# Optimization experiments

Hardware: AMD Instinct MI355X
Metric: run time of the kernel (lower is better)

## Reference

```python
import jax, jax.numpy as jnp
import numpy as np

B, NV, CIN, C = 1, 40000, 128, 64
D, H, W = 19, 200, 176  # sparse_shape = output_shape[1:4] + [1,0,0]
EPS = 1e-3
DN = ('NCDHW', 'OIDHW', 'NCDHW')


def setup_inputs():
    key = jax.random.key(0)
    ks = jax.random.split(key, 12)
    vf = jax.random.normal(ks[0], (NV, CIN), jnp.float32)
    bi = jnp.zeros((NV, 1), jnp.int32)
    zi = jax.random.randint(ks[1], (NV, 1), 0, D, jnp.int32)
    yi = jax.random.randint(ks[2], (NV, 1), 0, H, jnp.int32)
    xi = jax.random.randint(ks[3], (NV, 1), 0, W, jnp.int32)
    coors = jnp.concatenate([bi, zi, yi, xi], axis=1)  # [batch, z, y, x]
    s = 0.05
    w_sub1 = jax.random.normal(ks[4], (C, CIN, 3, 3, 3), jnp.float32) * s
    w_down1 = jax.random.normal(ks[5], (C, C, 3, 1, 1), jnp.float32) * s
    w_sub2 = jax.random.normal(ks[6], (C, C, 3, 3, 3), jnp.float32) * s
    w_sub3 = jax.random.normal(ks[7], (C, C, 3, 3, 3), jnp.float32) * s
    w_down2 = jax.random.normal(ks[8], (C, C, 3, 1, 1), jnp.float32) * s
    bn_gamma = 1.0 + 0.1 * jax.random.normal(ks[9], (5, C), jnp.float32)
    bn_beta = 0.1 * jax.random.normal(ks[10], (5, C), jnp.float32)
    bn_mean = 0.1 * jax.random.normal(ks[11], (5, C), jnp.float32)
    bn_var = jnp.ones((5, C), jnp.float32)
    return dict(voxel_features=vf, coors=coors, batch_size=1,
                w_sub1=w_sub1, w_down1=w_down1, w_sub2=w_sub2, w_sub3=w_sub3,
                w_down2=w_down2, bn_gamma=bn_gamma, bn_beta=bn_beta,
                bn_mean=bn_mean, bn_var=bn_var)


def _conv(x, w, stride, pad):
    return jax.lax.conv_general_dilated(x, w, stride, pad, dimension_numbers=DN)


def _bnrelu(x, i, mask, g, b, m, v):
    # eval-mode BN on active sites only (inactive sites stay exactly zero -> mask)
    inv = jax.lax.rsqrt(v[i] + EPS)
    y = (x - m[i][None, :, None, None, None]) * (g[i] * inv)[None, :, None, None, None] \
        + b[i][None, :, None, None, None]
    return jnp.maximum(y, 0.0) * mask


def _forward(voxel_features, coors, batch_size, w_sub1, w_down1, w_sub2, w_sub3,
             w_down2, bn_gamma, bn_beta, bn_mean, bn_var):
    bi, zi, yi, xi = coors[:, 0], coors[:, 1], coors[:, 2], coors[:, 3]
    # scn.InputLayer: scatter (sum duplicates) active voxel features into dense grid
    dense = jnp.zeros((batch_size, D, H, W, CIN), voxel_features.dtype)
    dense = dense.at[bi, zi, yi, xi].add(voxel_features)
    x = jnp.transpose(dense, (0, 4, 1, 2, 3))  # NCDHW
    mask = jnp.zeros((batch_size, D, H, W), voxel_features.dtype)
    mask = mask.at[bi, zi, yi, xi].set(1.0)[:, None]  # [B,1,D,H,W] active sites
    ones_k = jnp.ones((1, 1, 3, 1, 1), x.dtype)
    pad1 = ((1, 1), (1, 1), (1, 1))
    bn = (bn_gamma, bn_beta, bn_mean, bn_var)
    # SubmanifoldConvolution(128->64, k3) + BNReLU : output only at active sites
    x = _bnrelu(_conv(x, w_sub1, (1, 1, 1), pad1) * mask, 0, mask, *bn)
    # Convolution 64->64 kernel (3,1,1) stride (2,1,1): new active set = any input in window
    x = _conv(x, w_down1, (2, 1, 1), 'VALID')
    mask = (_conv(mask, ones_k, (2, 1, 1), 'VALID') > 0).astype(x.dtype)
    x = _bnrelu(x, 1, mask, *bn)
    # two more submanifold convs
    x = _bnrelu(_conv(x, w_sub2, (1, 1, 1), pad1) * mask, 2, mask, *bn)
    x = _bnrelu(_conv(x, w_sub3, (1, 1, 1), pad1) * mask, 3, mask, *bn)
    # second strided conv
    x = _conv(x, w_down2, (2, 1, 1), 'VALID')
    mask = (_conv(mask, ones_k, (2, 1, 1), 'VALID') > 0).astype(x.dtype)
    x = _bnrelu(x, 4, mask, *bn)
    # SparseToDense then view(N, C*D, H, W)
    Nb, Cc, Dd, Hh, Ww = x.shape
    return x.reshape(Nb, Cc * Dd, Hh, Ww)


def reference(voxel_features, coors, batch_size, w_sub1, w_down1, w_sub2, w_sub3,
              w_down2, bn_gamma, bn_beta, bn_mean, bn_var):
    return _forward(voxel_features, coors, batch_size, w_sub1, w_down1, w_sub2,
                    w_sub3, w_down2, bn_gamma, bn_beta, bn_mean, bn_var)
```

## Files before the change

kernel.cpp:

```cpp
#include <hip/hip_runtime.h>

typedef float floatx4 __attribute__((ext_vector_type(4)));
typedef _Float16 f16x8 __attribute__((ext_vector_type(8)));

#define D0_ 19
#define H0_ 200
#define W0_ 176
#define HW_ (H0_*W0_)
#define NCELL0 (D0_*HW_)
#define D1_ 9
#define NCELL1 (D1_*HW_)
#define D2_ 4
#define NCELL2 (D2_*HW_)
#define NV_ 40000
#define CAP0 40000
#define CAP1 80000
#define CAP2 140800
#define EPS_ 1e-3f

typedef __attribute__((address_space(1))) const unsigned int* gas_t;
typedef __attribute__((address_space(3))) unsigned int* las_t;

__device__ __forceinline__ short f2h(float f){
    _Float16 h = (_Float16)f;
    short s; __builtin_memcpy(&s, &h, 2); return s;
}

__device__ __forceinline__ void repack_one(const float* w, short* Bout, int i,
                                           int KCsrc, int kshift, int NSP){
    int k = i >> 6, n = i & 63;
    int j = k >> kshift;
    int ci = k & (KCsrc - 1);
    short val = f2h(w[(n * KCsrc + ci) * NSP + j]);
    int chunk = k >> 5, lanehi = (k >> 3) & 3, jj = k & 7;
    int nt = n >> 4, lane = lanehi * 16 + (n & 15);
    Bout[((chunk * 4 + nt) * 64 + lane) * 8 + jj] = val;
}

#define RP1 (3456*64)
#define RP2 (1728*64)
#define RPD (192*64)

__global__ void k_prep(const float* w1, const float* w2, const float* w3,
                       const float* wd1, const float* wd2,
                       short* B1, short* B2, short* B3, short* Bd1, short* Bd2,
                       const float* g, const float* b, const float* m, const float* v,
                       float* scale, float* shift){
    int i = blockIdx.x * 256 + threadIdx.x;
    if (i < RP1){ repack_one(w1, B1, i, 128, 7, 27); return; }
    i -= RP1;
    if (i < RP2){ repack_one(w2, B2, i, 64, 6, 27); return; }
    i -= RP2;
    if (i < RP2){ repack_one(w3, B3, i, 64, 6, 27); return; }
    i -= RP2;
    if (i < RPD){ repack_one(wd1, Bd1, i, 64, 6, 3); return; }
    i -= RPD;
    if (i < RPD){ repack_one(wd2, Bd2, i, 64, 6, 3); return; }
    i -= RPD;
    if (i < 5*64){
        float s = g[i] / sqrtf(v[i] + EPS_);
        scale[i] = s;
        shift[i] = b[i] - m[i] * s;
    }
}
#define PREP_TOT (RP1 + 2*RP2 + 2*RPD + 5*64)

__global__ void k_count(const int* coors, int* cntg){
    int v = blockIdx.x * 256 + threadIdx.x;
    if (v >= NV_) return;
    int z = coors[v*4+1], y = coors[v*4+2], x = coors[v*4+3];
    atomicAdd(&cntg[(z*H0_ + y)*W0_ + x], 1);
}

__device__ __forceinline__ int blk_rank(bool act, int* cnt, int& r_out){
    unsigned long long mask = __ballot(act);
    int lane = threadIdx.x & 63, wid = threadIdx.x >> 6;
    int wrank = __popcll(mask & ((1ull << lane) - 1));
    __shared__ int ws[4];
    __shared__ int blkbase;
    if (lane == 0) ws[wid] = __popcll(mask);
    __syncthreads();
    if (threadIdx.x == 0){
        int t0 = ws[0], t1 = ws[1], t2 = ws[2], t3 = ws[3];
        int tot = t0 + t1 + t2 + t3;
        blkbase = tot ? atomicAdd(cnt, tot) : 0;
        ws[0] = 0; ws[1] = t0; ws[2] = t0 + t1; ws[3] = t0 + t1 + t2;
    }
    __syncthreads();
    r_out = blkbase + ws[wid] + wrank;
    return 0;
}

__global__ void k_compact0(const int* cntg, int* idx0, int* list0, int* cnt0){
    int c = blockIdx.x * 256 + threadIdx.x;
    bool act = (c < NCELL0) && (cntg[c] > 0);
    int r; blk_rank(act, cnt0, r);
    if (c >= NCELL0) return;
    if (act){
        idx0[c] = r;
        int z = c / HW_; int rem = c - z * HW_;
        int y = rem / W0_; int x = rem - y * W0_;
        list0[r] = (z << 16) | (y << 8) | x;
    } else idx0[c] = -1;
}

__global__ void k_compact_dn(const int* idxsrc, int* idxdst, int* listdst, int* cnt,
                             int ncell){
    int c = blockIdx.x * 256 + threadIdx.x;
    bool act = false;
    int d = 0, y = 0, x = 0;
    if (c < ncell){
        d = c / HW_; int rem = c - d * HW_;
        y = rem / W0_; x = rem - y * W0_;
        #pragma unroll
        for (int j = 0; j < 3; ++j)
            act = act || (idxsrc[((2*d + j)*H0_ + y)*W0_ + x] >= 0);
    }
    int r; blk_rank(act, cnt, r);
    if (c >= ncell) return;
    if (act){
        idxdst[c] = r;
        listdst[r] = (d << 16) | (y << 8) | x;
    } else idxdst[c] = -1;
}

__global__ void k_scatter(const float* vf, const int* coors, const int* cntg,
                          const int* idx0, float* feat0f){
    int u = blockIdx.x * 256 + threadIdx.x;
    if (u >= NV_ * 32) return;
    int v = u >> 5, c4 = u & 31;
    int z = coors[v*4+1], y = coors[v*4+2], x = coors[v*4+3];
    int cell = (z*H0_ + y)*W0_ + x;
    int row = idx0[cell];
    float4 s = ((const float4*)(vf + (long)v * 128))[c4];
    float* dst = feat0f + (long)row * 128 + c4 * 4;
    if (cntg[cell] == 1){
        *(float4*)dst = s;
    } else {
        atomicAdd(dst+0, s.x); atomicAdd(dst+1, s.y);
        atomicAdd(dst+2, s.z); atomicAdd(dst+3, s.w);
    }
}

__global__ void k_convert(const float* f, short* b, const int* cntp){
    int n8 = cntp[0] * 16;
    int i = blockIdx.x * 256 + threadIdx.x;
    if (i >= n8) return;
    float4 a = ((const float4*)f)[i*2], c = ((const float4*)f)[i*2+1];
    short o[8] = { f2h(a.x), f2h(a.y), f2h(a.z), f2h(a.w),
                   f2h(c.x), f2h(c.y), f2h(c.z), f2h(c.w) };
    ((int4*)b)[i] = *(int4*)o;
}

__global__ void k_nbr27(const int* list0, const int* list1,
                        const int* idx0, const int* idx1,
                        int* nbr0T, int* nbr1T, const int* counters){
    int lvl = blockIdx.z;
    int j = blockIdx.y;
    int site = blockIdx.x * 256 + threadIdx.x;
    int M = counters[lvl];
    if (site >= M) return;
    const int* list = lvl ? list1 : list0;
    const int* idxg = lvl ? idx1 : idx0;
    int Dd = lvl ? D1_ : D0_;
    int cap = lvl ? CAP1 : CAP0;
    int cell = list[site];
    int z = cell >> 16, y = (cell >> 8) & 255, x = cell & 255;
    int nz = z + j/9 - 1, ny = y + (j/3)%3 - 1, nx = x + j%3 - 1;
    int r = -1;
    if ((unsigned)nz < (unsigned)Dd && (unsigned)ny < H0_ && (unsigned)nx < W0_)
        r = idxg[(nz*H0_ + ny)*W0_ + nx];
    (lvl ? nbr1T : nbr0T)[j * cap + site] = r;
}

__global__ void k_nbr3(const int* list1, const int* list2,
                       const int* idx0, const int* idx1,
                       int* dnb1T, int* dnb2T, const int* counters){
    int lvl = blockIdx.z;
    int j = blockIdx.y;
    int site = blockIdx.x * 256 + threadIdx.x;
    int M = counters[lvl + 1];
    if (site >= M) return;
    const int* list = lvl ? list2 : list1;
    const int* idxg = lvl ? idx1 : idx0;
    int cap = lvl ? CAP2 : CAP1;
    int cell = list[site];
    int d = cell >> 16, y = (cell >> 8) & 255, x = cell & 255;
    (lvl ? dnb2T : dnb1T)[j * cap + site] = idxg[((2*d + j)*H0_ + y)*W0_ + x];
}

template<int NNBR, int NCH, bool FINAL>
__global__ __launch_bounds__(256) void k_gemm(
    const short* __restrict__ featA, const int* __restrict__ nbrT, int nstride,
    const short* __restrict__ Bs, short* __restrict__ out,
    const int* __restrict__ cntp,
    const float* __restrict__ scale, const float* __restrict__ shift,
    const int* __restrict__ list, float* __restrict__ dout)
{
    __shared__ short Blds[2][NCH*4*512];
    int M = *cntp;
    int m0 = blockIdx.x * 128;
    if (m0 >= M) return;
    int tid = threadIdx.x;
    int wave = tid >> 6, lane = tid & 63;
    int m16 = lane & 15;
    int koff = (lane >> 4) * 8;
    const int ROWS = NCH * 32;

    int row0 = m0 + wave * 16 + m16;
    int row1 = row0 + 64;
    bool ok0 = row0 < M, ok1 = row1 < M;

    floatx4 acc0[4] = {}, acc1[4] = {};
    f16x8 A0[2][NCH], A1[2][NCH];
    const f16x8 z8 = {0,0,0,0,0,0,0,0};

    auto stageB = [&](int j, int b){
        #pragma unroll
        for (int f = 0; f < NCH; ++f){
            int frag = wave * NCH + f;
            const short* g = Bs + (((long)j * NCH * 4 + frag) * 64 + lane) * 8;
            __builtin_amdgcn_global_load_lds((gas_t)g, (las_t)&Blds[b][frag * 512],
                                             16, 0, 0);
        }
    };
    auto loadA1 = [&](f16x8* dst, int r, int kc){
        dst[kc] = (r >= 0) ? *(const f16x8*)(featA + (long)r*ROWS + koff + kc*32) : z8;
    };

    int rc0 = ok0 ? nbrT[row0] : -1;
    int rc1 = ok1 ? nbrT[row1] : -1;
    stageB(0, 0);
    #pragma unroll
    for (int kc = 0; kc < NCH; ++kc){ loadA1(A0[0], rc0, kc); loadA1(A1[0], rc1, kc); }
    int rb0 = (NNBR > 1 && ok0) ? nbrT[nstride + row0] : -1;
    int rb1 = (NNBR > 1 && ok1) ? nbrT[nstride + row1] : -1;
    int ra0 = -1, ra1 = -1;
    __syncthreads();

    #pragma unroll
    for (int t = 0; t < NNBR; ++t){
        if (t + 1 < NNBR){
            stageB(t + 1, (t + 1) & 1);
            #pragma unroll
            for (int kc = 0; kc < NCH; ++kc){ loadA1(A0[(t+1)&1], rb0, kc); loadA1(A1[(t+1)&1], rb1, kc); }
        }
        if (t + 2 < NNBR){
            ra0 = ok0 ? nbrT[(t+2)*nstride + row0] : -1;
            ra1 = ok1 ? nbrT[(t+2)*nstride + row1] : -1;
        }
        const short* Bb = Blds[t & 1];
        #pragma unroll
        for (int kc = 0; kc < NCH; ++kc){
            f16x8 b[4];
            #pragma unroll
            for (int nt = 0; nt < 4; ++nt)
                b[nt] = *(const f16x8*)&Bb[((kc*4 + nt) * 64 + lane) * 8];
            f16x8 a0 = A0[t&1][kc], a1 = A1[t&1][kc];
            #pragma unroll
            for (int nt = 0; nt < 4; ++nt)
                acc0[nt] = __builtin_amdgcn_mfma_f32_16x16x32_f16(a0, b[nt], acc0[nt], 0, 0, 0);
            #pragma unroll
            for (int nt = 0; nt < 4; ++nt)
                acc1[nt] = __builtin_amdgcn_mfma_f32_16x16x32_f16(a1, b[nt], acc1[nt], 0, 0, 0);
        }
        rb0 = ra0; rb1 = ra1;
        __syncthreads();
    }

    int n16 = lane & 15;
    #pragma unroll
    for (int rg = 0; rg < 2; ++rg){
        const floatx4* ac = rg ? acc1 : acc0;
        int mb = m0 + (wave + rg*4) * 16 + (lane >> 4) * 4;
        #pragma unroll
        for (int nt = 0; nt < 4; ++nt){
            int n = nt * 16 + n16;
            float sc = scale[n], sh = shift[n];
            #pragma unroll
            for (int r = 0; r < 4; ++r){
                int site = mb + r;
                if (site < M){
                    float y = fmaxf(ac[nt][r] * sc + sh, 0.f);
                    if (FINAL){
                        int cell = list[site];
                        int d = cell >> 16, yy = (cell >> 8) & 255, xx = cell & 255;
                        dout[((n*4 + d)*H0_ + yy)*W0_ + xx] = y;
                    } else {
                        out[(long)site*64 + n] = f2h(y);
                    }
                }
            }
        }
    }
}

extern "C" void kernel_launch(void* const* d_in, const int* in_sizes, int n_in,
                              void* d_out, int out_size, void* d_ws, size_t ws_size,
                              hipStream_t stream){
    const float* vf   = (const float*)d_in[0];
    const int*   coors= (const int*)  d_in[1];
    const float* w1   = (const float*)d_in[3];
    const float* wd1  = (const float*)d_in[4];
    const float* w2   = (const float*)d_in[5];
    const float* w3   = (const float*)d_in[6];
    const float* wd2  = (const float*)d_in[7];
    const float* bng  = (const float*)d_in[8];
    const float* bnb  = (const float*)d_in[9];
    const float* bnm  = (const float*)d_in[10];
    const float* bnv  = (const float*)d_in[11];
    float* dout = (float*)d_out;

    char* ws = (char*)d_ws;
    size_t off = 0;
    auto alloc = [&](size_t bytes)->char* {
        char* p = ws + off;
        off += (bytes + 255) & ~(size_t)255;
        return p;
    };

    int*   counters = (int*)  alloc(256);
    int*   cntg     = (int*)  alloc((size_t)NCELL0 * 4);
    int*   idx0     = (int*)  alloc((size_t)NCELL0 * 4);
    int*   idx1     = (int*)  alloc((size_t)NCELL1 * 4);
    int*   idx2     = (int*)  alloc((size_t)NCELL2 * 4);
    int*   list0    = (int*)  alloc((size_t)CAP0 * 4);
    int*   list1    = (int*)  alloc((size_t)CAP1 * 4);
    int*   list2    = (int*)  alloc((size_t)CAP2 * 4);
    float* feat0f   = (float*)alloc((size_t)CAP0 * 128 * 4);
    short* feat0h   = (short*)alloc((size_t)CAP0 * 128 * 2);
    short* feat1    = (short*)alloc((size_t)CAP0 * 64 * 2);
    short* featd1   = (short*)alloc((size_t)CAP1 * 64 * 2);
    short* feat2    = (short*)alloc((size_t)CAP1 * 64 * 2);
    short* feat3    = (short*)alloc((size_t)CAP1 * 64 * 2);
    int*   nbr0T    = (int*)  alloc((size_t)CAP0 * 27 * 4);
    int*   nbr1T    = (int*)  alloc((size_t)CAP1 * 27 * 4);
    int*   dnb1T    = (int*)  alloc((size_t)CAP1 * 3 * 4);
    int*   dnb2T    = (int*)  alloc((size_t)CAP2 * 3 * 4);
    short* B1  = (short*)alloc((size_t)3456 * 64 * 2);
    short* B2  = (short*)alloc((size_t)1728 * 64 * 2);
    short* B3  = (short*)alloc((size_t)1728 * 64 * 2);
    short* Bd1 = (short*)alloc((size_t)192 * 64 * 2);
    short* Bd2 = (short*)alloc((size_t)192 * 64 * 2);
    float* bnscale = (float*)alloc(5 * 64 * 4);
    float* bnshift = (float*)alloc(5 * 64 * 4);

    hipMemsetAsync(counters, 0, 256 + (size_t)NCELL0 * 4, stream);
    hipMemsetAsync(feat0f, 0, (size_t)CAP0 * 128 * 4, stream);
    hipMemsetAsync(dout, 0, (size_t)out_size * 4, stream);

    k_prep<<<(PREP_TOT + 255)/256, 256, 0, stream>>>(w1, w2, w3, wd1, wd2,
        B1, B2, B3, Bd1, Bd2, bng, bnb, bnm, bnv, bnscale, bnshift);

    k_count<<<(NV_ + 255)/256, 256, 0, stream>>>(coors, cntg);
    k_compact0<<<(NCELL0 + 255)/256, 256, 0, stream>>>(cntg, idx0, list0, counters + 0);
    k_scatter<<<(NV_*32 + 255)/256, 256, 0, stream>>>(vf, coors, cntg, idx0, feat0f);
    k_convert<<<(CAP0*16 + 255)/256, 256, 0, stream>>>(feat0f, feat0h, counters + 0);
    k_compact_dn<<<(NCELL1 + 255)/256, 256, 0, stream>>>(idx0, idx1, list1, counters + 1, NCELL1);
    k_compact_dn<<<(NCELL2 + 255)/256, 256, 0, stream>>>(idx1, idx2, list2, counters + 2, NCELL2);

    dim3 g27((CAP1 + 255)/256, 27, 2);
    k_nbr27<<<g27, 256, 0, stream>>>(list0, list1, idx0, idx1, nbr0T, nbr1T, counters);
    dim3 g3((CAP2 + 255)/256, 3, 2);
    k_nbr3<<<g3, 256, 0, stream>>>(list1, list2, idx0, idx1, dnb1T, dnb2T, counters);

    k_gemm<27,4,false><<<(CAP0+127)/128, 256, 0, stream>>>(feat0h, nbr0T, CAP0, B1, feat1,
        counters + 0, bnscale + 0,   bnshift + 0,   nullptr, nullptr);
    k_gemm<3,2,false><<<(CAP1+127)/128, 256, 0, stream>>>(feat1, dnb1T, CAP1, Bd1, featd1,
        counters + 1, bnscale + 64,  bnshift + 64,  nullptr, nullptr);
    k_gemm<27,2,false><<<(CAP1+127)/128, 256, 0, stream>>>(featd1, nbr1T, CAP1, B2, feat2,
        counters + 1, bnscale + 128, bnshift + 128, nullptr, nullptr);
    k_gemm<27,2,false><<<(CAP1+127)/128, 256, 0, stream>>>(feat2, nbr1T, CAP1, B3, feat3,
        counters + 1, bnscale + 192, bnshift + 192, nullptr, nullptr);
    k_gemm<3,2,true><<<(CAP2+127)/128, 256, 0, stream>>>(feat3, dnb2T, CAP2, Bd2, nullptr,
        counters + 2, bnscale + 256, bnshift + 256, list2, dout);
}
```

Baseline: 322.1 us.

## Halve gemm row tile, skip MFMAs for all-empty neighbor offsets, merge nbr kernels

The sparse-conv gemm now processes 64 rows per block (one 16-row group per wave) instead of 128, which doubles the grid and cuts register pressure. Each wave skips the MFMA work for a neighbor offset when no lane in the wave has a valid neighbor, using a ballot. The two neighbor-table kernels are merged into one launch. In exchange, each block reuses the staged weights over half as many rows and issues twice as many weight stages in total. The merged neighbor grid also launches many blocks that exit early.

```diff
diff --git a/kernel.cpp b/kernel.cpp
--- a/kernel.cpp
+++ b/kernel.cpp
@@ -152,41 +152,39 @@
     ((int4*)b)[i] = *(int4*)o;
 }
 
-__global__ void k_nbr27(const int* list0, const int* list1,
-                        const int* idx0, const int* idx1,
-                        int* nbr0T, int* nbr1T, const int* counters){
-    int lvl = blockIdx.z;
+__global__ void k_nbrs(const int* list0, const int* list1, const int* list2,
+                       const int* idx0, const int* idx1,
+                       int* nbr0T, int* nbr1T, int* dnb1T, int* dnb2T,
+                       const int* counters){
+    int job = blockIdx.z;
     int j = blockIdx.y;
     int site = blockIdx.x * 256 + threadIdx.x;
-    int M = counters[lvl];
-    if (site >= M) return;
-    const int* list = lvl ? list1 : list0;
-    const int* idxg = lvl ? idx1 : idx0;
-    int Dd = lvl ? D1_ : D0_;
-    int cap = lvl ? CAP1 : CAP0;
-    int cell = list[site];
-    int z = cell >> 16, y = (cell >> 8) & 255, x = cell & 255;
-    int nz = z + j/9 - 1, ny = y + (j/3)%3 - 1, nx = x + j%3 - 1;
-    int r = -1;
-    if ((unsigned)nz < (unsigned)Dd && (unsigned)ny < H0_ && (unsigned)nx < W0_)
-        r = idxg[(nz*H0_ + ny)*W0_ + nx];
-    (lvl ? nbr1T : nbr0T)[j * cap + site] = r;
-}
-
-__global__ void k_nbr3(const int* list1, const int* list2,
-                       const int* idx0, const int* idx1,
-                       int* dnb1T, int* dnb2T, const int* counters){
-    int lvl = blockIdx.z;
-    int j = blockIdx.y;
-    int site = blockIdx.x * 256 + threadIdx.x;
-    int M = counters[lvl + 1];
-    if (site >= M) return;
-    const int* list = lvl ? list2 : list1;
-    const int* idxg = lvl ? idx1 : idx0;
-    int cap = lvl ? CAP2 : CAP1;
-    int cell = list[site];
-    int d = cell >> 16, y = (cell >> 8) & 255, x = cell & 255;
-    (lvl ? dnb2T : dnb1T)[j * cap + site] = idxg[((2*d + j)*H0_ + y)*W0_ + x];
+    if (job < 2){
+        int M = counters[job];
+        if (site >= M) return;
+        const int* list = job ? list1 : list0;
+        const int* idxg = job ? idx1 : idx0;
+        int Dd = job ? D1_ : D0_;
+        int cap = job ? CAP1 : CAP0;
+        int cell = list[site];
+        int z = cell >> 16, y = (cell >> 8) & 255, x = cell & 255;
+        int nz = z + j/9 - 1, ny = y + (j/3)%3 - 1, nx = x + j%3 - 1;
+        int r = -1;
+        if ((unsigned)nz < (unsigned)Dd && (unsigned)ny < H0_ && (unsigned)nx < W0_)
+            r = idxg[(nz*H0_ + ny)*W0_ + nx];
+        (job ? nbr1T : nbr0T)[j * cap + site] = r;
+    } else {
+        if (j >= 3) return;
+        int lvl = job - 2;
+        int M = counters[lvl + 1];
+        if (site >= M) return;
+        const int* list = lvl ? list2 : list1;
+        const int* idxg = lvl ? idx1 : idx0;
+        int cap = lvl ? CAP2 : CAP1;
+        int cell = list[site];
+        int d = cell >> 16, y = (cell >> 8) & 255, x = cell & 255;
+        (lvl ? dnb2T : dnb1T)[j * cap + site] = idxg[((2*d + j)*H0_ + y)*W0_ + x];
+    }
 }
 
 template<int NNBR, int NCH, bool FINAL>
@@ -199,26 +197,26 @@
 {
     __shared__ short Blds[2][NCH*4*512];
     int M = *cntp;
-    int m0 = blockIdx.x * 128;
+    int m0 = blockIdx.x * 64;
     if (m0 >= M) return;
     int tid = threadIdx.x;
     int wave = tid >> 6, lane = tid & 63;
     int m16 = lane & 15;
     int koff = (lane >> 4) * 8;
     const int ROWS = NCH * 32;
-
-    int row0 = m0 + wave * 16 + m16;
-    int row1 = row0 + 64;
-    bool ok0 = row0 < M, ok1 = row1 < M;
-
-    floatx4 acc0[4] = {}, acc1[4] = {};
-    f16x8 A0[2][NCH], A1[2][NCH];
+    const int FPW = NCH;
+
+    int row = m0 + wave * 16 + m16;
+    bool ok = row < M;
+
+    floatx4 acc[4] = {};
+    f16x8 A[2][NCH];
     const f16x8 z8 = {0,0,0,0,0,0,0,0};
 
     auto stageB = [&](int j, int b){
         #pragma unroll
-        for (int f = 0; f < NCH; ++f){
-            int frag = wave * NCH + f;
+        for (int f = 0; f < FPW; ++f){
+            int frag = wave * FPW + f;
             const short* g = Bs + (((long)j * NCH * 4 + frag) * 64 + lane) * 8;
             __builtin_amdgcn_global_load_lds((gas_t)g, (las_t)&Blds[b][frag * 512],
                                              16, 0, 0);
@@ -228,14 +226,12 @@
         dst[kc] = (r >= 0) ? *(const f16x8*)(featA + (long)r*ROWS + koff + kc*32) : z8;
     };
 
-    int rc0 = ok0 ? nbrT[row0] : -1;
-    int rc1 = ok1 ? nbrT[row1] : -1;
+    int rc = ok ? nbrT[row] : -1;
     stageB(0, 0);
     #pragma unroll
-    for (int kc = 0; kc < NCH; ++kc){ loadA1(A0[0], rc0, kc); loadA1(A1[0], rc1, kc); }
-    int rb0 = (NNBR > 1 && ok0) ? nbrT[nstride + row0] : -1;
-    int rb1 = (NNBR > 1 && ok1) ? nbrT[nstride + row1] : -1;
-    int ra0 = -1, ra1 = -1;
+    for (int kc = 0; kc < NCH; ++kc) loadA1(A[0], rc, kc);
+    int rb = (NNBR > 1 && ok) ? nbrT[nstride + row] : -1;
+    int ra = -1;
     __syncthreads();
 
     #pragma unroll
@@ -243,52 +239,45 @@
         if (t + 1 < NNBR){
             stageB(t + 1, (t + 1) & 1);
             #pragma unroll
-            for (int kc = 0; kc < NCH; ++kc){ loadA1(A0[(t+1)&1], rb0, kc); loadA1(A1[(t+1)&1], rb1, kc); }
+            for (int kc = 0; kc < NCH; ++kc) loadA1(A[(t+1)&1], rb, kc);
         }
-        if (t + 2 < NNBR){
-            ra0 = ok0 ? nbrT[(t+2)*nstride + row0] : -1;
-            ra1 = ok1 ? nbrT[(t+2)*nstride + row1] : -1;
+        if (t + 2 < NNBR)
+            ra = ok ? nbrT[(t+2)*nstride + row] : -1;
+        if (__ballot(rc >= 0) != 0){
+            const short* Bb = Blds[t & 1];
+            #pragma unroll
+            for (int kc = 0; kc < NCH; ++kc){
+                f16x8 b[4];
+                #pragma unroll
+                for (int nt = 0; nt < 4; ++nt)
+                    b[nt] = *(const f16x8*)&Bb[((kc*4 + nt) * 64 + lane) * 8];
+                f16x8 a = A[t&1][kc];
+                #pragma unroll
+                for (int nt = 0; nt < 4; ++nt)
+                    acc[nt] = __builtin_amdgcn_mfma_f32_16x16x32_f16(a, b[nt], acc[nt], 0, 0, 0);
+            }
         }
-        const short* Bb = Blds[t & 1];
+        rc = rb; rb = ra;
+        __syncthreads();
+    }
+
+    int n16 = lane & 15;
+    int mb = m0 + wave * 16 + (lane >> 4) * 4;
+    #pragma unroll
+    for (int nt = 0; nt < 4; ++nt){
+        int n = nt * 16 + n16;
+        float sc = scale[n], sh = shift[n];
         #pragma unroll
-        for (int kc = 0; kc < NCH; ++kc){
-            f16x8 b[4];
-            #pragma unroll
-            for (int nt = 0; nt < 4; ++nt)
-                b[nt] = *(const f16x8*)&Bb[((kc*4 + nt) * 64 + lane) * 8];
-            f16x8 a0 = A0[t&1][kc], a1 = A1[t&1][kc];
-            #pragma unroll
-            for (int nt = 0; nt < 4; ++nt)
-                acc0[nt] = __builtin_amdgcn_mfma_f32_16x16x32_f16(a0, b[nt], acc0[nt], 0, 0, 0);
-            #pragma unroll
-            for (int nt = 0; nt < 4; ++nt)
-                acc1[nt] = __builtin_amdgcn_mfma_f32_16x16x32_f16(a1, b[nt], acc1[nt], 0, 0, 0);
-        }
-        rb0 = ra0; rb1 = ra1;
-        __syncthreads();
-    }
-
-    int n16 = lane & 15;
-    #pragma unroll
-    for (int rg = 0; rg < 2; ++rg){
-        const floatx4* ac = rg ? acc1 : acc0;
-        int mb = m0 + (wave + rg*4) * 16 + (lane >> 4) * 4;
-        #pragma unroll
-        for (int nt = 0; nt < 4; ++nt){
-            int n = nt * 16 + n16;
-            float sc = scale[n], sh = shift[n];
-            #pragma unroll
-            for (int r = 0; r < 4; ++r){
-                int site = mb + r;
-                if (site < M){
-                    float y = fmaxf(ac[nt][r] * sc + sh, 0.f);
-                    if (FINAL){
-                        int cell = list[site];
-                        int d = cell >> 16, yy = (cell >> 8) & 255, xx = cell & 255;
-                        dout[((n*4 + d)*H0_ + yy)*W0_ + xx] = y;
-                    } else {
-                        out[(long)site*64 + n] = f2h(y);
-                    }
+        for (int r = 0; r < 4; ++r){
+            int site = mb + r;
+            if (site < M){
+                float y = fmaxf(acc[nt][r] * sc + sh, 0.f);
+                if (FINAL){
+                    int cell = list[site];
+                    int d = cell >> 16, yy = (cell >> 8) & 255, xx = cell & 255;
+                    dout[((n*4 + d)*H0_ + yy)*W0_ + xx] = y;
+                } else {
+                    out[(long)site*64 + n] = f2h(y);
                 }
             }
         }
@@ -359,19 +348,18 @@
     k_compact_dn<<<(NCELL1 + 255)/256, 256, 0, stream>>>(idx0, idx1, list1, counters + 1, NCELL1);
     k_compact_dn<<<(NCELL2 + 255)/256, 256, 0, stream>>>(idx1, idx2, list2, counters + 2, NCELL2);
 
-    dim3 g27((CAP1 + 255)/256, 27, 2);
-    k_nbr27<<<g27, 256, 0, stream>>>(list0, list1, idx0, idx1, nbr0T, nbr1T, counters);
-    dim3 g3((CAP2 + 255)/256, 3, 2);
-    k_nbr3<<<g3, 256, 0, stream>>>(list1, list2, idx0, idx1, dnb1T, dnb2T, counters);
-
-    k_gemm<27,4,false><<<(CAP0+127)/128, 256, 0, stream>>>(feat0h, nbr0T, CAP0, B1, feat1,
+    dim3 gn((CAP2 + 255)/256, 27, 4);
+    k_nbrs<<<gn, 256, 0, stream>>>(list0, list1, list2, idx0, idx1,
+                                   nbr0T, nbr1T, dnb1T, dnb2T, counters);
+
+    k_gemm<27,4,false><<<(CAP0+63)/64, 256, 0, stream>>>(feat0h, nbr0T, CAP0, B1, feat1,
         counters + 0, bnscale + 0,   bnshift + 0,   nullptr, nullptr);
-    k_gemm<3,2,false><<<(CAP1+127)/128, 256, 0, stream>>>(feat1, dnb1T, CAP1, Bd1, featd1,
+    k_gemm<3,2,false><<<(CAP1+63)/64, 256, 0, stream>>>(feat1, dnb1T, CAP1, Bd1, featd1,
         counters + 1, bnscale + 64,  bnshift + 64,  nullptr, nullptr);
-    k_gemm<27,2,false><<<(CAP1+127)/128, 256, 0, stream>>>(featd1, nbr1T, CAP1, B2, feat2,
+    k_gemm<27,2,false><<<(CAP1+63)/64, 256, 0, stream>>>(featd1, nbr1T, CAP1, B2, feat2,
         counters + 1, bnscale + 128, bnshift + 128, nullptr, nullptr);
-    k_gemm<27,2,false><<<(CAP1+127)/128, 256, 0, stream>>>(feat2, nbr1T, CAP1, B3, feat3,
+    k_gemm<27,2,false><<<(CAP1+63)/64, 256, 0, stream>>>(feat2, nbr1T, CAP1, B3, feat3,
         counters + 1, bnscale + 192, bnshift + 192, nullptr, nullptr);
-    k_gemm<3,2,true><<<(CAP2+127)/128, 256, 0, stream>>>(feat3, dnb2T, CAP2, Bd2, nullptr,
+    k_gemm<3,2,true><<<(CAP2+63)/64, 256, 0, stream>>>(feat3, dnb2T, CAP2, Bd2, nullptr,
         counters + 2, bnscale + 256, bnshift + 256, list2, dout);
 }
```

New measurement: 318.0 us. No clear change (-1.3%).
